# Kernel optimization log

Hardware: AMD Instinct MI355X
Metric: run time of the kernel (lower is better)

## Reference

```python
import jax, jax.numpy as jnp
import numpy as np

N_NODES = 50000

def _spmm(edge_index, edge_weight, feat):
    # adj @ feat where adj is given as COO edge list (dst <- src)
    src = edge_index[1]
    dst = edge_index[0]
    msgs = feat[src] * edge_weight[:, None]  # [E, F]
    return jax.ops.segment_sum(msgs, dst, num_segments=N_NODES)

def setup_inputs() -> dict:
    key = jax.random.key(0)
    ks = jax.random.split(key, 8)
    E = 1600000
    x = jax.random.normal(ks[0], (N_NODES, 512), dtype=jnp.float32)
    edge_index = jax.random.randint(ks[1], (2, E), 0, N_NODES, dtype=jnp.int32)
    edge_weight = jax.random.uniform(ks[2], (E,), dtype=jnp.float32)
    # Glorot-ish init like GraphConvolution.reset_parameters
    W1 = jax.random.normal(ks[3], (512, 128), dtype=jnp.float32) / np.sqrt(512)
    b1 = jax.random.normal(ks[4], (128,), dtype=jnp.float32) * 0.01
    W2 = jax.random.normal(ks[5], (128, 64), dtype=jnp.float32) / np.sqrt(128)
    b2 = jax.random.normal(ks[6], (64,), dtype=jnp.float32) * 0.01
    return {"x": x, "edge_index": edge_index, "edge_weight": edge_weight,
            "W1": W1, "b1": b1, "W2": W2, "b2": b2}

def reference(x, edge_index, edge_weight, W1, b1, W2, b2):
    # eval mode: F.dropout is identity when not training
    # gc1: adj @ (x @ W1) + b1, then relu
    support1 = x @ W1                                   # [N, nhid]
    x1 = jax.nn.relu(_spmm(edge_index, edge_weight, support1) + b1)
    # gc2: adj @ (x1 @ W2) + b2
    support2 = x1 @ W2                                  # [N, out]
    x2 = _spmm(edge_index, edge_weight, support2) + b2
    return (x1, x2)
```

## Files before the change

kernel.cpp:

```cpp
#include <hip/hip_runtime.h>
#include <hip/hip_bf16.h>

#define N_NODES 50000
#define N_EDGES 1600000
#define F_IN    512
#define F_HID   128
#define F_OUT   64
#define NBUK    391
#define EPB     2048
#define CAP     4864

typedef short bf16x8 __attribute__((ext_vector_type(8)));
typedef float f32x4  __attribute__((ext_vector_type(4)));

__device__ __forceinline__ short f32_to_bf16(float f) {
    unsigned u = __float_as_uint(f);
    u += 0x7FFF + ((u >> 16) & 1);
    return (short)(u >> 16);
}
__device__ __forceinline__ float bf16_to_f32(short s) {
    return __uint_as_float(((unsigned)(unsigned short)s) << 16);
}
__device__ __forceinline__ float bf16lo(unsigned u) { return __uint_as_float(u << 16); }
__device__ __forceinline__ float bf16hi(unsigned u) { return __uint_as_float(u & 0xFFFF0000u); }

__device__ __forceinline__ bf16x8 cvt8(float4 lo, float4 hi) {
    union { unsigned u[4]; bf16x8 v; } r;
    asm("v_cvt_pk_bf16_f32 %0, %1, %2" : "=v"(r.u[0]) : "v"(lo.x), "v"(lo.y));
    asm("v_cvt_pk_bf16_f32 %0, %1, %2" : "=v"(r.u[1]) : "v"(lo.z), "v"(lo.w));
    asm("v_cvt_pk_bf16_f32 %0, %1, %2" : "=v"(r.u[2]) : "v"(hi.x), "v"(hi.y));
    asm("v_cvt_pk_bf16_f32 %0, %1, %2" : "=v"(r.u[3]) : "v"(hi.z), "v"(hi.w));
    return r.v;
}

__device__ __forceinline__ void gload16(const void* g, void* l) {
    __builtin_amdgcn_global_load_lds((const __attribute__((address_space(1))) void*)g,
                                     (__attribute__((address_space(3))) void*)l, 16, 0, 0);
}


__global__ __launch_bounds__(256) void part_a(const int* __restrict__ dst,
                                              const int* __restrict__ src,
                                              const float* __restrict__ w,
                                              int* __restrict__ gcnt,
                                              uint2* __restrict__ tmp, int E) {
    __shared__ int h[NBUK];
    __shared__ int base_[NBUK];
    __shared__ int ex[NBUK];
    __shared__ int curz[NBUK];
    __shared__ int   ldst[EPB];
    __shared__ uint2 rec[EPB];
    __shared__ int   tgt[EPB];
    const int tid = threadIdx.x;
    for (int i = tid; i < NBUK; i += 256) { h[i] = 0; curz[i] = 0; }
    __syncthreads();
    int e0 = blockIdx.x * EPB;
    int e1 = min(e0 + EPB, E);
    int cnt = e1 - e0;
    for (int e = e0 + tid; e < e1; e += 256) {
        int d = dst[e];
        ldst[e - e0] = d;
        atomicAdd(&h[d >> 7], 1);
    }
    __syncthreads();
    for (int i = tid; i < NBUK; i += 256) {
        int c = h[i];
        base_[i] = c ? atomicAdd(&gcnt[i], c) : 0;
        ex[i] = c;
    }
    __syncthreads();
    for (int off = 1; off < NBUK; off <<= 1) {
        int i0 = tid, i1 = tid + 256;
        int t0 = 0, t1 = 0;
        if (i0 < NBUK && i0 >= off) t0 = ex[i0 - off];
        if (i1 < NBUK && i1 >= off) t1 = ex[i1 - off];
        __syncthreads();
        if (i0 < NBUK && i0 >= off) ex[i0] += t0;
        if (i1 < NBUK && i1 >= off) ex[i1] += t1;
        __syncthreads();
    }
    for (int e = e0 + tid; e < e1; e += 256) {
        int d = ldst[e - e0];
        int b = d >> 7;
        int j0 = atomicAdd(&curz[b], 1);
        int slot = ex[b] - h[b] + j0;
        rec[slot] = make_uint2(((unsigned)d << 16) | (unsigned)src[e],
                               __float_as_uint(w[e]));
        int goff = base_[b] + j0;
        tgt[slot] = (goff < CAP) ? b * CAP + goff : -1;
    }
    __syncthreads();
    for (int i = tid; i < cnt; i += 256) {
        int t = tgt[i];
        if (t >= 0) tmp[t] = rec[i];
    }
}

__global__ __launch_bounds__(256) void part_b(const uint2* __restrict__ tmp,
                                              const int* __restrict__ gcnt,
                                              int2* __restrict__ rowinfo,
                                              uint2* __restrict__ erec) {
    __shared__ int s[128];
    __shared__ int cur[128];
    __shared__ uint2 rec[CAP];
    __shared__ uint2 ord[CAP];
    int b = blockIdx.x, tid = threadIdx.x;
    int nb0 = b << 7;
    int r0 = b * CAP;
    int cnt_b = min(gcnt[b], CAP);
    if (tid < 128) s[tid] = 0;
    __syncthreads();
    for (int i = tid; i < cnt_b; i += 256) {
        uint2 r = tmp[r0 + i];
        rec[i] = r;
        atomicAdd(&s[(r.x >> 16) - nb0], 1);
    }
    __syncthreads();
    int v = (tid < 128) ? s[tid] : 0;
    #pragma unroll
    for (int off = 1; off < 128; off <<= 1) {
        int t = (tid >= off && tid < 128) ? s[tid - off] : 0;
        __syncthreads();
        if (tid < 128) s[tid] += t;
        __syncthreads();
    }
    if (tid < 128) {
        int ex = s[tid] - v;
        cur[tid] = ex;
        int node = nb0 + tid;
        if (node < N_NODES) rowinfo[node] = make_int2(r0 + ex, r0 + ex + v);
    }
    __syncthreads();
    for (int i = tid; i < cnt_b; i += 256) {
        uint2 r = rec[i];
        int p = atomicAdd(&cur[(r.x >> 16) - nb0], 1);
        ord[p] = make_uint2(r.x & 0xFFFFu, r.y);
    }
    __syncthreads();
    for (int i = tid; i < cnt_b; i += 256)
        erec[r0 + i] = ord[i];
}


template<int KD, int NC>
__device__ __forceinline__ void wtrans_one(const float* __restrict__ W,
                                           bf16x8* __restrict__ Bfrag, int u) {
    constexpr int NT = NC / 16;
    int lane = u & 63;
    int nt   = (u >> 6) % NT;
    int kc   = u / (64 * NT);
    int n = nt * 16 + (lane & 15);
    int k = kc * 32 + (lane >> 4) * 8;
    bf16x8 f;
    #pragma unroll
    for (int j = 0; j < 8; ++j) f[j] = f32_to_bf16(W[(size_t)(k + j) * NC + n]);
    Bfrag[u] = f;
}

__global__ __launch_bounds__(256) void wtrans_all(const float* __restrict__ W1,
                                                  const float* __restrict__ W2,
                                                  bf16x8* __restrict__ B1,
                                                  bf16x8* __restrict__ B2) {
    constexpr int U1 = (F_IN / 32) * (F_HID / 16) * 64;
    constexpr int U2 = (F_HID / 32) * (F_OUT / 16) * 64;
    int u = blockIdx.x * 256 + threadIdx.x;
    if (u < U1) wtrans_one<F_IN, F_HID>(W1, B1, u);
    else if (u < U1 + U2) wtrans_one<F_HID, F_OUT>(W2, B2, u - U1);
}

template<int KD , int NC >
__global__ __launch_bounds__(256) void mfma_gemm_s1(const float* __restrict__ X,
                                                    const bf16x8* __restrict__ Bfrag,
                                                    short* __restrict__ C, int Mrows) {
    constexpr int S = KD / 32;
    __shared__ char lds[3][16384];
    const int tid  = threadIdx.x;
    const int lane = tid & 63;
    const int wave = tid >> 6;
    const int wm = wave >> 1, wn = wave & 1;
    const int B0 = blockIdx.x * 64;
    const int r_lo = lane & 15, cg = lane >> 4;

    int rowA = B0 + wave * 16 + r_lo;
    if (rowA > Mrows - 1) rowA = Mrows - 1;
    const char* gA = (const char*)(X + (size_t)rowA * KD) + cg * 32;
    const char* gB = (const char*)Bfrag + (size_t)(wave * 2) * 1024 + (size_t)lane * 16;

    const int dA0 = (0 * 256 + wave * 64) * 16;
    const int dA1 = (1 * 256 + wave * 64) * 16;
    const int dB0 = 8192 + (wave * 2 + 0) * 1024;
    const int dB1 = 8192 + (wave * 2 + 1) * 1024;

    f32x4 acc[2][4];
    #pragma unroll
    for (int m = 0; m < 2; ++m)
        #pragma unroll
        for (int n = 0; n < 4; ++n) acc[m][n] = (f32x4){0.f, 0.f, 0.f, 0.f};

    auto issue_stage = [&](int s, char* L) {
        const char* a = gA + (size_t)s * 128;
        const char* b = gB + (size_t)s * 8192;
        gload16(a,        L + dA0);
        gload16(a + 16,   L + dA1);
        gload16(b,        L + dB0);
        gload16(b + 1024, L + dB1);
    };
    auto compute_step = [&](const char* L) {
        const char* A_ = L;
        const char* B_ = L + 8192;
        bf16x8 bb[4];
        #pragma unroll
        for (int n = 0; n < 4; ++n)
            bb[n] = *(const bf16x8*)(B_ + (wn * 4 + n) * 1024 + lane * 16);
        #pragma unroll
        for (int m = 0; m < 2; ++m) {
            int t = wm * 2 + m;
            float4 lo = *(const float4*)(A_ + (0 * 256 + t * 64 + lane) * 16);
            float4 hi = *(const float4*)(A_ + (1 * 256 + t * 64 + lane) * 16);
            bf16x8 a = cvt8(lo, hi);
            #pragma unroll
            for (int n = 0; n < 4; ++n)
                acc[m][n] = __builtin_amdgcn_mfma_f32_16x16x32_bf16(a, bb[n], acc[m][n], 0, 0, 0);
        }
    };

    issue_stage(0, lds[0]);
    issue_stage(1, lds[1]);
    issue_stage(2, lds[2]);

    for (int s = 0; s < S - 2; ++s) {
        asm volatile("s_waitcnt vmcnt(8)" ::: "memory");
        asm volatile("s_barrier" ::: "memory");
        compute_step(lds[s % 3]);
        asm volatile("s_barrier" ::: "memory");
        if (s + 3 < S) issue_stage(s + 3, lds[s % 3]);
    }
    asm volatile("s_waitcnt vmcnt(4)" ::: "memory");
    asm volatile("s_barrier" ::: "memory");
    compute_step(lds[(S - 2) % 3]);
    asm volatile("s_waitcnt vmcnt(0)" ::: "memory");
    asm volatile("s_barrier" ::: "memory");
    compute_step(lds[(S - 1) % 3]);

    #pragma unroll
    for (int m = 0; m < 2; ++m) {
        int tile16 = (B0 >> 4) + wm * 2 + m;
        if (tile16 * 16 < Mrows) {
            #pragma unroll
            for (int n = 0; n < 4; ++n) {
                #pragma unroll
                for (int r = 0; r < 4; ++r) {
                    int grow = tile16 * 16 + cg * 4 + r;
                    C[(size_t)grow * NC + (wn * 4 + n) * 16 + r_lo] = f32_to_bf16(acc[m][n][r]);
                }
            }
        }
    }
}


template<int NC, int KD>
__global__ __launch_bounds__(256) void mfma_gemm_frag(const bf16x8* __restrict__ Afrag,
                                                      const bf16x8* __restrict__ Bfrag,
                                                      short* __restrict__ C, int Mt) {
    constexpr int NT = NC / 16, KC = KD / 32;
    constexpr int PFA = (KC < 4) ? KC : 4;
    const int lane = threadIdx.x & 63;
    const int wave = threadIdx.x >> 6;
    const int tile = blockIdx.x * 4 + wave;
    if (tile >= Mt) return;

    const bf16x8* ap = Afrag + (size_t)tile * KC * 64 + lane;
    const bf16x8* bp = Bfrag + lane;

    f32x4 acc[NT];
    #pragma unroll
    for (int i = 0; i < NT; ++i) acc[i] = (f32x4){0.f, 0.f, 0.f, 0.f};

    bf16x8 abuf[PFA];
    #pragma unroll
    for (int i = 0; i < PFA; ++i) abuf[i] = ap[(size_t)i * 64];
    bf16x8 bbuf[NT];
    #pragma unroll
    for (int nt = 0; nt < NT; ++nt) bbuf[nt] = bp[(size_t)nt * 64];

    #pragma unroll
    for (int kc = 0; kc < KC; ++kc) {
        bf16x8 a = abuf[kc % PFA];
        int ka = kc + PFA; if (ka > KC - 1) ka = KC - 1;
        abuf[kc % PFA] = ap[(size_t)ka * 64];
        int kb = (kc + 1 < KC) ? kc + 1 : kc;
        bf16x8 bnew[NT];
        #pragma unroll
        for (int nt = 0; nt < NT; ++nt) {
            bnew[nt] = bp[((size_t)kb * NT + nt) * 64];
            acc[nt] = __builtin_amdgcn_mfma_f32_16x16x32_bf16(a, bbuf[nt], acc[nt], 0, 0, 0);
        }
        #pragma unroll
        for (int nt = 0; nt < NT; ++nt) bbuf[nt] = bnew[nt];
    }

    const int lrow = lane & 15, kgrp = lane >> 4;
    #pragma unroll
    for (int nt = 0; nt < NT; ++nt) {
        #pragma unroll
        for (int r = 0; r < 4; ++r) {
            int grow = tile * 16 + kgrp * 4 + r;
            C[(size_t)grow * NC + nt * 16 + lrow] = f32_to_bf16(acc[nt][r]);
        }
    }
}


__global__ __launch_bounds__(64) void spmm128(const int2* __restrict__ rowinfo,
                                              const uint2* __restrict__ erec,
                                              const unsigned* __restrict__ featu,
                                              const float* __restrict__ bias,
                                              float* __restrict__ out,
                                              unsigned* __restrict__ afrag2u) {
    int d = blockIdx.x, tid = threadIdx.x;
    int2 ri = rowinfo[d];
    int beg = ri.x, end = ri.y;
    float a0 = 0.f, a1 = 0.f;
    const unsigned* fp = featu + tid;
    int e = beg;
    if (end - beg >= 8) {
        uint2 r[8];
        #pragma unroll
        for (int j = 0; j < 8; ++j) r[j] = erec[e + j];
        for (; e + 16 <= end; e += 8) {
            unsigned f[8];
            #pragma unroll
            for (int j = 0; j < 8; ++j) f[j] = fp[r[j].x * 64u];
            uint2 rn[8];
            #pragma unroll
            for (int j = 0; j < 8; ++j) rn[j] = erec[e + 8 + j];
            #pragma unroll
            for (int j = 0; j < 8; ++j) {
                float w = __uint_as_float(r[j].y);
                a0 += w * bf16lo(f[j]);
                a1 += w * bf16hi(f[j]);
            }
            #pragma unroll
            for (int j = 0; j < 8; ++j) r[j] = rn[j];
        }
        {
            unsigned f[8];
            #pragma unroll
            for (int j = 0; j < 8; ++j) f[j] = fp[r[j].x * 64u];
            #pragma unroll
            for (int j = 0; j < 8; ++j) {
                float w = __uint_as_float(r[j].y);
                a0 += w * bf16lo(f[j]);
                a1 += w * bf16hi(f[j]);
            }
            e += 8;
        }
    }
    for (; e + 4 <= end; e += 4) {
        uint2 r0 = erec[e], r1 = erec[e + 1], r2 = erec[e + 2], r3 = erec[e + 3];
        unsigned f0 = fp[r0.x * 64u];
        unsigned f1 = fp[r1.x * 64u];
        unsigned f2 = fp[r2.x * 64u];
        unsigned f3 = fp[r3.x * 64u];
        float w0 = __uint_as_float(r0.y), w1 = __uint_as_float(r1.y);
        float w2 = __uint_as_float(r2.y), w3 = __uint_as_float(r3.y);
        a0 += w0 * bf16lo(f0); a1 += w0 * bf16hi(f0);
        a0 += w1 * bf16lo(f1); a1 += w1 * bf16hi(f1);
        a0 += w2 * bf16lo(f2); a1 += w2 * bf16hi(f2);
        a0 += w3 * bf16lo(f3); a1 += w3 * bf16hi(f3);
    }
    for (; e < end; ++e) {
        uint2 r = erec[e];
        unsigned f = fp[r.x * 64u];
        float w = __uint_as_float(r.y);
        a0 += w * bf16lo(f); a1 += w * bf16hi(f);
    }
    float ox = fmaxf(a0 + bias[2 * tid], 0.f);
    float oy = fmaxf(a1 + bias[2 * tid + 1], 0.f);
    *(float2*)&out[(size_t)d * 128 + 2 * tid] = make_float2(ox, oy);
    unsigned packed = (unsigned)(unsigned short)f32_to_bf16(ox) |
                      ((unsigned)(unsigned short)f32_to_bf16(oy) << 16);
    int unit = ((d >> 4) * 4 + (tid >> 4)) * 64 + ((tid >> 2) & 3) * 16 + (d & 15);
    afrag2u[unit * 4 + (tid & 3)] = packed;
}

__global__ __launch_bounds__(64) void spmm64(const int2* __restrict__ rowinfo,
                                             const uint2* __restrict__ erec,
                                             const short* __restrict__ feat,
                                             const float* __restrict__ bias,
                                             float* __restrict__ out) {
    int d = blockIdx.x, tid = threadIdx.x;
    int2 ri = rowinfo[d];
    int beg = ri.x, end = ri.y;
    float acc = 0.f;
    const short* fp = feat + tid;
    int e = beg;
    if (end - beg >= 8) {
        uint2 r[8];
        #pragma unroll
        for (int j = 0; j < 8; ++j) r[j] = erec[e + j];
        for (; e + 16 <= end; e += 8) {
            float f[8];
            #pragma unroll
            for (int j = 0; j < 8; ++j) f[j] = bf16_to_f32(fp[r[j].x * 64u]);
            uint2 rn[8];
            #pragma unroll
            for (int j = 0; j < 8; ++j) rn[j] = erec[e + 8 + j];
            #pragma unroll
            for (int j = 0; j < 8; ++j) acc += __uint_as_float(r[j].y) * f[j];
            #pragma unroll
            for (int j = 0; j < 8; ++j) r[j] = rn[j];
        }
        {
            float f[8];
            #pragma unroll
            for (int j = 0; j < 8; ++j) f[j] = bf16_to_f32(fp[r[j].x * 64u]);
            #pragma unroll
            for (int j = 0; j < 8; ++j) acc += __uint_as_float(r[j].y) * f[j];
            e += 8;
        }
    }
    for (; e + 4 <= end; e += 4) {
        uint2 r0 = erec[e], r1 = erec[e + 1], r2 = erec[e + 2], r3 = erec[e + 3];
        float f0 = bf16_to_f32(fp[r0.x * 64u]);
        float f1 = bf16_to_f32(fp[r1.x * 64u]);
        float f2 = bf16_to_f32(fp[r2.x * 64u]);
        float f3 = bf16_to_f32(fp[r3.x * 64u]);
        acc += __uint_as_float(r0.y) * f0;
        acc += __uint_as_float(r1.y) * f1;
        acc += __uint_as_float(r2.y) * f2;
        acc += __uint_as_float(r3.y) * f3;
    }
    for (; e < end; ++e) {
        uint2 r = erec[e];
        acc += __uint_as_float(r.y) * bf16_to_f32(fp[r.x * 64u]);
    }
    out[(size_t)d * 64 + tid] = acc + bias[tid];
}


extern "C" void kernel_launch(void* const* d_in, const int* in_sizes, int n_in,
                              void* d_out, int out_size, void* d_ws, size_t ws_size,
                              hipStream_t stream) {
    const float* x  = (const float*)d_in[0];
    const int*   ei = (const int*)d_in[1];
    const float* ew = (const float*)d_in[2];
    const float* W1 = (const float*)d_in[3];
    const float* b1 = (const float*)d_in[4];
    const float* W2 = (const float*)d_in[5];
    const float* b2 = (const float*)d_in[6];

    const int* dst = ei;
    const int* src = ei + N_EDGES;

    float* x1 = (float*)d_out;
    float* x2 = x1 + (size_t)N_NODES * F_HID;

    char* ws = (char*)d_ws;
    uint2*  erec     = (uint2*)ws;  ws += (size_t)NBUK * CAP * 8;
    uint2*  tmp      = (uint2*)ws;  ws += (size_t)NBUK * CAP * 8;
    short*  support1 = (short*)ws;  ws += (size_t)N_NODES * F_HID * 2;
    short*  support2 = (short*)ws;  ws += (size_t)N_NODES * F_OUT * 2;
    bf16x8* Afrag2   = (bf16x8*)ws; ws += (size_t)N_NODES * F_HID * 2;
    bf16x8* Bfrag1   = (bf16x8*)ws; ws += (size_t)F_HID * F_IN * 2;
    bf16x8* Bfrag2   = (bf16x8*)ws; ws += (size_t)F_OUT * F_HID * 2;
    int2*   rowinfo  = (int2*)ws;   ws += (size_t)N_NODES * 8;
    int*    gcnt     = (int*)ws;    ws += 400 * 4;

    const int NPB = (N_EDGES + EPB - 1) / EPB;
    const int MT  = N_NODES / 16;

    hipMemsetAsync(gcnt, 0, NBUK * sizeof(int), stream);
    part_a<<<NPB, 256, 0, stream>>>(dst, src, ew, gcnt, tmp, N_EDGES);
    part_b<<<NBUK, 256, 0, stream>>>(tmp, gcnt, rowinfo, erec);

    wtrans_all<<<36, 256, 0, stream>>>(W1, W2, Bfrag1, Bfrag2);

    {
        int blocks = (N_NODES + 63) / 64;
        mfma_gemm_s1<F_IN, F_HID><<<blocks, 256, 0, stream>>>(x, Bfrag1, support1, N_NODES);
    }

    spmm128<<<N_NODES, 64, 0, stream>>>(rowinfo, erec, (const unsigned*)support1, b1, x1,
                                        (unsigned*)Afrag2);

    mfma_gemm_frag<F_OUT, F_HID><<<(MT + 3) / 4, 256, 0, stream>>>(Afrag2, Bfrag2, support2, MT);

    spmm64<<<N_NODES, 64, 0, stream>>>(rowinfo, erec, support2, b2, x2);
}
```

Before: 333.0 us.

## Merge independent preprocessing and GEMM kernels into two horizontally fused launches

Folds the edge bucketing pass (part_a) and the weight fragment transform into one launch, dispatching on block index. It likewise folds the per-bucket CSR sort (part_b) and the first dense GEMM into one launch that shares a 48KB LDS arena. part_b now re-reads tmp from global memory instead of caching it in LDS. The aim is to cut launch gaps and let the independent sort and GEMM blocks overlap on the GPU. The cost is higher LDS allocation for the sort blocks, and the sort path pays a second global read of its records.

```diff
diff --git a/kernel.cpp b/kernel.cpp
--- a/kernel.cpp
+++ b/kernel.cpp
@@ -9,6 +9,7 @@
 #define NBUK    391
 #define EPB     2048
 #define CAP     4864
+#define NPB_A   ((N_EDGES + EPB - 1) / EPB)
 
 typedef short bf16x8 __attribute__((ext_vector_type(8)));
 typedef float f32x4  __attribute__((ext_vector_type(4)));
@@ -37,110 +38,6 @@
     __builtin_amdgcn_global_load_lds((const __attribute__((address_space(1))) void*)g,
                                      (__attribute__((address_space(3))) void*)l, 16, 0, 0);
 }
-
-
-__global__ __launch_bounds__(256) void part_a(const int* __restrict__ dst,
-                                              const int* __restrict__ src,
-                                              const float* __restrict__ w,
-                                              int* __restrict__ gcnt,
-                                              uint2* __restrict__ tmp, int E) {
-    __shared__ int h[NBUK];
-    __shared__ int base_[NBUK];
-    __shared__ int ex[NBUK];
-    __shared__ int curz[NBUK];
-    __shared__ int   ldst[EPB];
-    __shared__ uint2 rec[EPB];
-    __shared__ int   tgt[EPB];
-    const int tid = threadIdx.x;
-    for (int i = tid; i < NBUK; i += 256) { h[i] = 0; curz[i] = 0; }
-    __syncthreads();
-    int e0 = blockIdx.x * EPB;
-    int e1 = min(e0 + EPB, E);
-    int cnt = e1 - e0;
-    for (int e = e0 + tid; e < e1; e += 256) {
-        int d = dst[e];
-        ldst[e - e0] = d;
-        atomicAdd(&h[d >> 7], 1);
-    }
-    __syncthreads();
-    for (int i = tid; i < NBUK; i += 256) {
-        int c = h[i];
-        base_[i] = c ? atomicAdd(&gcnt[i], c) : 0;
-        ex[i] = c;
-    }
-    __syncthreads();
-    for (int off = 1; off < NBUK; off <<= 1) {
-        int i0 = tid, i1 = tid + 256;
-        int t0 = 0, t1 = 0;
-        if (i0 < NBUK && i0 >= off) t0 = ex[i0 - off];
-        if (i1 < NBUK && i1 >= off) t1 = ex[i1 - off];
-        __syncthreads();
-        if (i0 < NBUK && i0 >= off) ex[i0] += t0;
-        if (i1 < NBUK && i1 >= off) ex[i1] += t1;
-        __syncthreads();
-    }
-    for (int e = e0 + tid; e < e1; e += 256) {
-        int d = ldst[e - e0];
-        int b = d >> 7;
-        int j0 = atomicAdd(&curz[b], 1);
-        int slot = ex[b] - h[b] + j0;
-        rec[slot] = make_uint2(((unsigned)d << 16) | (unsigned)src[e],
-                               __float_as_uint(w[e]));
-        int goff = base_[b] + j0;
-        tgt[slot] = (goff < CAP) ? b * CAP + goff : -1;
-    }
-    __syncthreads();
-    for (int i = tid; i < cnt; i += 256) {
-        int t = tgt[i];
-        if (t >= 0) tmp[t] = rec[i];
-    }
-}
-
-__global__ __launch_bounds__(256) void part_b(const uint2* __restrict__ tmp,
-                                              const int* __restrict__ gcnt,
-                                              int2* __restrict__ rowinfo,
-                                              uint2* __restrict__ erec) {
-    __shared__ int s[128];
-    __shared__ int cur[128];
-    __shared__ uint2 rec[CAP];
-    __shared__ uint2 ord[CAP];
-    int b = blockIdx.x, tid = threadIdx.x;
-    int nb0 = b << 7;
-    int r0 = b * CAP;
-    int cnt_b = min(gcnt[b], CAP);
-    if (tid < 128) s[tid] = 0;
-    __syncthreads();
-    for (int i = tid; i < cnt_b; i += 256) {
-        uint2 r = tmp[r0 + i];
-        rec[i] = r;
-        atomicAdd(&s[(r.x >> 16) - nb0], 1);
-    }
-    __syncthreads();
-    int v = (tid < 128) ? s[tid] : 0;
-    #pragma unroll
-    for (int off = 1; off < 128; off <<= 1) {
-        int t = (tid >= off && tid < 128) ? s[tid - off] : 0;
-        __syncthreads();
-        if (tid < 128) s[tid] += t;
-        __syncthreads();
-    }
-    if (tid < 128) {
-        int ex = s[tid] - v;
-        cur[tid] = ex;
-        int node = nb0 + tid;
-        if (node < N_NODES) rowinfo[node] = make_int2(r0 + ex, r0 + ex + v);
-    }
-    __syncthreads();
-    for (int i = tid; i < cnt_b; i += 256) {
-        uint2 r = rec[i];
-        int p = atomicAdd(&cur[(r.x >> 16) - nb0], 1);
-        ord[p] = make_uint2(r.x & 0xFFFFu, r.y);
-    }
-    __syncthreads();
-    for (int i = tid; i < cnt_b; i += 256)
-        erec[r0 + i] = ord[i];
-}
-
 
 template<int KD, int NC>
 __device__ __forceinline__ void wtrans_one(const float* __restrict__ W,
@@ -157,101 +54,203 @@
     Bfrag[u] = f;
 }
 
-__global__ __launch_bounds__(256) void wtrans_all(const float* __restrict__ W1,
-                                                  const float* __restrict__ W2,
-                                                  bf16x8* __restrict__ B1,
-                                                  bf16x8* __restrict__ B2) {
-    constexpr int U1 = (F_IN / 32) * (F_HID / 16) * 64;
-    constexpr int U2 = (F_HID / 32) * (F_OUT / 16) * 64;
-    int u = blockIdx.x * 256 + threadIdx.x;
-    if (u < U1) wtrans_one<F_IN, F_HID>(W1, B1, u);
-    else if (u < U1 + U2) wtrans_one<F_HID, F_OUT>(W2, B2, u - U1);
-}
-
-template<int KD , int NC >
-__global__ __launch_bounds__(256) void mfma_gemm_s1(const float* __restrict__ X,
-                                                    const bf16x8* __restrict__ Bfrag,
-                                                    short* __restrict__ C, int Mrows) {
-    constexpr int S = KD / 32;
-    __shared__ char lds[3][16384];
-    const int tid  = threadIdx.x;
-    const int lane = tid & 63;
-    const int wave = tid >> 6;
-    const int wm = wave >> 1, wn = wave & 1;
-    const int B0 = blockIdx.x * 64;
-    const int r_lo = lane & 15, cg = lane >> 4;
-
-    int rowA = B0 + wave * 16 + r_lo;
-    if (rowA > Mrows - 1) rowA = Mrows - 1;
-    const char* gA = (const char*)(X + (size_t)rowA * KD) + cg * 32;
-    const char* gB = (const char*)Bfrag + (size_t)(wave * 2) * 1024 + (size_t)lane * 16;
-
-    const int dA0 = (0 * 256 + wave * 64) * 16;
-    const int dA1 = (1 * 256 + wave * 64) * 16;
-    const int dB0 = 8192 + (wave * 2 + 0) * 1024;
-    const int dB1 = 8192 + (wave * 2 + 1) * 1024;
-
-    f32x4 acc[2][4];
-    #pragma unroll
-    for (int m = 0; m < 2; ++m)
-        #pragma unroll
-        for (int n = 0; n < 4; ++n) acc[m][n] = (f32x4){0.f, 0.f, 0.f, 0.f};
-
-    auto issue_stage = [&](int s, char* L) {
-        const char* a = gA + (size_t)s * 128;
-        const char* b = gB + (size_t)s * 8192;
-        gload16(a,        L + dA0);
-        gload16(a + 16,   L + dA1);
-        gload16(b,        L + dB0);
-        gload16(b + 1024, L + dB1);
-    };
-    auto compute_step = [&](const char* L) {
-        const char* A_ = L;
-        const char* B_ = L + 8192;
-        bf16x8 bb[4];
-        #pragma unroll
-        for (int n = 0; n < 4; ++n)
-            bb[n] = *(const bf16x8*)(B_ + (wn * 4 + n) * 1024 + lane * 16);
+
+__global__ __launch_bounds__(256) void fused_aw(const int* __restrict__ dst,
+                                                const int* __restrict__ src,
+                                                const float* __restrict__ w,
+                                                int* __restrict__ gcnt,
+                                                uint2* __restrict__ tmp, int E,
+                                                const float* __restrict__ W1,
+                                                const float* __restrict__ W2,
+                                                bf16x8* __restrict__ B1,
+                                                bf16x8* __restrict__ B2) {
+    const int tid = threadIdx.x;
+    if (blockIdx.x < NPB_A) {
+        __shared__ int h[NBUK];
+        __shared__ int base_[NBUK];
+        __shared__ int ex[NBUK];
+        __shared__ int curz[NBUK];
+        __shared__ int   ldst[EPB];
+        __shared__ uint2 rec[EPB];
+        __shared__ int   tgt[EPB];
+        for (int i = tid; i < NBUK; i += 256) { h[i] = 0; curz[i] = 0; }
+        __syncthreads();
+        int e0 = blockIdx.x * EPB;
+        int e1 = min(e0 + EPB, E);
+        int cnt = e1 - e0;
+        for (int e = e0 + tid; e < e1; e += 256) {
+            int d = dst[e];
+            ldst[e - e0] = d;
+            atomicAdd(&h[d >> 7], 1);
+        }
+        __syncthreads();
+        for (int i = tid; i < NBUK; i += 256) {
+            int c = h[i];
+            base_[i] = c ? atomicAdd(&gcnt[i], c) : 0;
+            ex[i] = c;
+        }
+        __syncthreads();
+        for (int off = 1; off < NBUK; off <<= 1) {
+            int i0 = tid, i1 = tid + 256;
+            int t0 = 0, t1 = 0;
+            if (i0 < NBUK && i0 >= off) t0 = ex[i0 - off];
+            if (i1 < NBUK && i1 >= off) t1 = ex[i1 - off];
+            __syncthreads();
+            if (i0 < NBUK && i0 >= off) ex[i0] += t0;
+            if (i1 < NBUK && i1 >= off) ex[i1] += t1;
+            __syncthreads();
+        }
+        for (int e = e0 + tid; e < e1; e += 256) {
+            int d = ldst[e - e0];
+            int b = d >> 7;
+            int j0 = atomicAdd(&curz[b], 1);
+            int slot = ex[b] - h[b] + j0;
+            rec[slot] = make_uint2(((unsigned)d << 16) | (unsigned)src[e],
+                                   __float_as_uint(w[e]));
+            int goff = base_[b] + j0;
+            tgt[slot] = (goff < CAP) ? b * CAP + goff : -1;
+        }
+        __syncthreads();
+        for (int i = tid; i < cnt; i += 256) {
+            int t = tgt[i];
+            if (t >= 0) tmp[t] = rec[i];
+        }
+    } else {
+        constexpr int U1 = (F_IN / 32) * (F_HID / 16) * 64;
+        constexpr int U2 = (F_HID / 32) * (F_OUT / 16) * 64;
+        int u = (blockIdx.x - NPB_A) * 256 + tid;
+        if (u < U1) wtrans_one<F_IN, F_HID>(W1, B1, u);
+        else if (u < U1 + U2) wtrans_one<F_HID, F_OUT>(W2, B2, u - U1);
+    }
+}
+
+
+__global__ __launch_bounds__(256) void fused_bg(const uint2* __restrict__ tmp,
+                                                const int* __restrict__ gcnt,
+                                                int2* __restrict__ rowinfo,
+                                                uint2* __restrict__ erec,
+                                                const float* __restrict__ X,
+                                                const bf16x8* __restrict__ Bfrag,
+                                                short* __restrict__ C, int Mrows) {
+    __shared__ char arena[49152];
+    const int tid = threadIdx.x;
+    if (blockIdx.x < NBUK) {
+        int* s   = (int*)arena;
+        int* cur = (int*)(arena + 512);
+        uint2* ord = (uint2*)(arena + 1024);
+        int b = blockIdx.x;
+        int nb0 = b << 7;
+        int r0 = b * CAP;
+        int cnt_b = min(gcnt[b], CAP);
+        if (tid < 128) s[tid] = 0;
+        __syncthreads();
+        for (int i = tid; i < cnt_b; i += 256)
+            atomicAdd(&s[(tmp[r0 + i].x >> 16) - nb0], 1);
+        __syncthreads();
+        int v = (tid < 128) ? s[tid] : 0;
+        #pragma unroll
+        for (int off = 1; off < 128; off <<= 1) {
+            int t = (tid >= off && tid < 128) ? s[tid - off] : 0;
+            __syncthreads();
+            if (tid < 128) s[tid] += t;
+            __syncthreads();
+        }
+        if (tid < 128) {
+            int ex = s[tid] - v;
+            cur[tid] = ex;
+            int node = nb0 + tid;
+            if (node < N_NODES) rowinfo[node] = make_int2(r0 + ex, r0 + ex + v);
+        }
+        __syncthreads();
+        for (int i = tid; i < cnt_b; i += 256) {
+            uint2 r = tmp[r0 + i];
+            int p = atomicAdd(&cur[(r.x >> 16) - nb0], 1);
+            ord[p] = make_uint2(r.x & 0xFFFFu, r.y);
+        }
+        __syncthreads();
+        for (int i = tid; i < cnt_b; i += 256)
+            erec[r0 + i] = ord[i];
+    } else {
+        constexpr int KD = F_IN, NC = F_HID;
+        constexpr int S = KD / 32;
+        const int lane = tid & 63;
+        const int wave = tid >> 6;
+        const int wm = wave >> 1, wn = wave & 1;
+        const int B0 = (blockIdx.x - NBUK) * 64;
+        const int r_lo = lane & 15, cg = lane >> 4;
+
+        int rowA = B0 + wave * 16 + r_lo;
+        if (rowA > Mrows - 1) rowA = Mrows - 1;
+        const char* gA = (const char*)(X + (size_t)rowA * KD) + cg * 32;
+        const char* gB = (const char*)Bfrag + (size_t)(wave * 2) * 1024 + (size_t)lane * 16;
+
+        const int dA0 = (0 * 256 + wave * 64) * 16;
+        const int dA1 = (1 * 256 + wave * 64) * 16;
+        const int dB0 = 8192 + (wave * 2 + 0) * 1024;
+        const int dB1 = 8192 + (wave * 2 + 1) * 1024;
+
+        f32x4 acc[2][4];
+        #pragma unroll
+        for (int m = 0; m < 2; ++m)
+            #pragma unroll
+            for (int n = 0; n < 4; ++n) acc[m][n] = (f32x4){0.f, 0.f, 0.f, 0.f};
+
+        auto issue_stage = [&](int s_, char* L) {
+            const char* a = gA + (size_t)s_ * 128;
+            const char* b = gB + (size_t)s_ * 8192;
+            gload16(a,        L + dA0);
+            gload16(a + 16,   L + dA1);
+            gload16(b,        L + dB0);
+            gload16(b + 1024, L + dB1);
+        };
+        auto compute_step = [&](const char* L) {
+            const char* A_ = L;
+            const char* B_ = L + 8192;
+            bf16x8 bb[4];
+            #pragma unroll
+            for (int n = 0; n < 4; ++n)
+                bb[n] = *(const bf16x8*)(B_ + (wn * 4 + n) * 1024 + lane * 16);
+            #pragma unroll
+            for (int m = 0; m < 2; ++m) {
+                int t = wm * 2 + m;
+                float4 lo = *(const float4*)(A_ + (0 * 256 + t * 64 + lane) * 16);
+                float4 hi = *(const float4*)(A_ + (1 * 256 + t * 64 + lane) * 16);
+                bf16x8 a = cvt8(lo, hi);
+                #pragma unroll
+                for (int n = 0; n < 4; ++n)
+                    acc[m][n] = __builtin_amdgcn_mfma_f32_16x16x32_bf16(a, bb[n], acc[m][n], 0, 0, 0);
+            }
+        };
+
+        issue_stage(0, arena);
+        issue_stage(1, arena + 16384);
+        issue_stage(2, arena + 32768);
+
+        for (int s_ = 0; s_ < S - 2; ++s_) {
+            asm volatile("s_waitcnt vmcnt(8)" ::: "memory");
+            asm volatile("s_barrier" ::: "memory");
+            compute_step(arena + (s_ % 3) * 16384);
+            asm volatile("s_barrier" ::: "memory");
+            if (s_ + 3 < S) issue_stage(s_ + 3, arena + (s_ % 3) * 16384);
+        }
+        asm volatile("s_waitcnt vmcnt(4)" ::: "memory");
+        asm volatile("s_barrier" ::: "memory");
+        compute_step(arena + ((S - 2) % 3) * 16384);
+        asm volatile("s_waitcnt vmcnt(0)" ::: "memory");
+        asm volatile("s_barrier" ::: "memory");
+        compute_step(arena + ((S - 1) % 3) * 16384);
+
         #pragma unroll
         for (int m = 0; m < 2; ++m) {
-            int t = wm * 2 + m;
-            float4 lo = *(const float4*)(A_ + (0 * 256 + t * 64 + lane) * 16);
-            float4 hi = *(const float4*)(A_ + (1 * 256 + t * 64 + lane) * 16);
-            bf16x8 a = cvt8(lo, hi);
-            #pragma unroll
-            for (int n = 0; n < 4; ++n)
-                acc[m][n] = __builtin_amdgcn_mfma_f32_16x16x32_bf16(a, bb[n], acc[m][n], 0, 0, 0);
-        }
-    };
-
-    issue_stage(0, lds[0]);
-    issue_stage(1, lds[1]);
-    issue_stage(2, lds[2]);
-
-    for (int s = 0; s < S - 2; ++s) {
-        asm volatile("s_waitcnt vmcnt(8)" ::: "memory");
-        asm volatile("s_barrier" ::: "memory");
-        compute_step(lds[s % 3]);
-        asm volatile("s_barrier" ::: "memory");
-        if (s + 3 < S) issue_stage(s + 3, lds[s % 3]);
-    }
-    asm volatile("s_waitcnt vmcnt(4)" ::: "memory");
-    asm volatile("s_barrier" ::: "memory");
-    compute_step(lds[(S - 2) % 3]);
-    asm volatile("s_waitcnt vmcnt(0)" ::: "memory");
-    asm volatile("s_barrier" ::: "memory");
-    compute_step(lds[(S - 1) % 3]);
-
-    #pragma unroll
-    for (int m = 0; m < 2; ++m) {
-        int tile16 = (B0 >> 4) + wm * 2 + m;
-        if (tile16 * 16 < Mrows) {
-            #pragma unroll
-            for (int n = 0; n < 4; ++n) {
+            int tile16 = (B0 >> 4) + wm * 2 + m;
+            if (tile16 * 16 < Mrows) {
                 #pragma unroll
-                for (int r = 0; r < 4; ++r) {
-                    int grow = tile16 * 16 + cg * 4 + r;
-                    C[(size_t)grow * NC + (wn * 4 + n) * 16 + r_lo] = f32_to_bf16(acc[m][n][r]);
+                for (int n = 0; n < 4; ++n) {
+                    #pragma unroll
+                    for (int r = 0; r < 4; ++r) {
+                        int grow = tile16 * 16 + cg * 4 + r;
+                        C[(size_t)grow * NC + (wn * 4 + n) * 16 + r_lo] = f32_to_bf16(acc[m][n][r]);
+                    }
                 }
             }
         }
@@ -468,19 +467,15 @@
     int2*   rowinfo  = (int2*)ws;   ws += (size_t)N_NODES * 8;
     int*    gcnt     = (int*)ws;    ws += 400 * 4;
 
-    const int NPB = (N_EDGES + EPB - 1) / EPB;
-    const int MT  = N_NODES / 16;
+    const int MT = N_NODES / 16;
+    const int GB = (N_NODES + 63) / 64;
 
     hipMemsetAsync(gcnt, 0, NBUK * sizeof(int), stream);
-    part_a<<<NPB, 256, 0, stream>>>(dst, src, ew, gcnt, tmp, N_EDGES);
-    part_b<<<NBUK, 256, 0, stream>>>(tmp, gcnt, rowinfo, erec);
-
-    wtrans_all<<<36, 256, 0, stream>>>(W1, W2, Bfrag1, Bfrag2);
-
-    {
-        int blocks = (N_NODES + 63) / 64;
-        mfma_gemm_s1<F_IN, F_HID><<<blocks, 256, 0, stream>>>(x, Bfrag1, support1, N_NODES);
-    }
+    fused_aw<<<NPB_A + 36, 256, 0, stream>>>(dst, src, ew, gcnt, tmp, N_EDGES,
+                                             W1, W2, Bfrag1, Bfrag2);
+
+    fused_bg<<<NBUK + GB, 256, 0, stream>>>(tmp, gcnt, rowinfo, erec,
+                                            x, Bfrag1, support1, N_NODES);
 
     spmm128<<<N_NODES, 64, 0, stream>>>(rowinfo, erec, (const unsigned*)support1, b1, x1,
                                         (unsigned*)Afrag2);
```

Result: faster. 315.2 us (-5.3%).
